# Kernel optimization log

Measured on AMD Instinct MI355X. Metric: run time of the kernel, lower is better.

Reference implementation:

```python
import jax, jax.numpy as jnp
import numpy as np

B, N, K = 4, 1024, 32
C_S, C_Z, C_H, H, PQ, PV = 384, 128, 16, 12, 4, 8
INF, EPS = 1e5, 1e-8
LN_EPS = 1e-5


def _quat_to_rot(q):
    # q: [..., 4] unit quaternions -> [..., 3, 3]
    w, x, y, z = q[..., 0], q[..., 1], q[..., 2], q[..., 3]
    r = jnp.stack([
        1 - 2 * (y * y + z * z), 2 * (x * y - w * z), 2 * (x * z + w * y),
        2 * (x * y + w * z), 1 - 2 * (x * x + z * z), 2 * (y * z - w * x),
        2 * (x * z - w * y), 2 * (y * z + w * x), 1 - 2 * (x * x + y * y),
    ], axis=-1)
    return r.reshape(q.shape[:-1] + (3, 3))


def _layernorm(x, scale, bias):
    m = jnp.mean(x, axis=-1, keepdims=True)
    v = jnp.mean((x - m) ** 2, axis=-1, keepdims=True)
    return (x - m) * jax.lax.rsqrt(v + LN_EPS) * scale + bias


def setup_inputs():
    key = jax.random.key(0)
    ks = jax.random.split(key, 16)
    s = jax.random.normal(ks[0], (B, N, C_S), jnp.float32)
    z = jax.random.normal(ks[1], (B, N, K, C_Z), jnp.float32)
    edge_index = jax.random.randint(ks[2], (B, N, K), 0, N, jnp.int32)
    quat = jax.random.normal(ks[3], (B, N, 4), jnp.float32)
    rot = _quat_to_rot(quat / jnp.linalg.norm(quat, axis=-1, keepdims=True))
    trans = 10.0 * jax.random.normal(ks[4], (B, N, 3), jnp.float32)
    s_mask = jnp.ones((B, N), jnp.float32)
    sc_s, sc_z = C_S ** -0.5, C_Z ** -0.5
    return {
        "s": s, "z": z, "edge_index": edge_index, "rot": rot, "trans": trans,
        "s_mask": s_mask,
        "ln_s_scale": jnp.ones((C_S,), jnp.float32),
        "ln_s_bias": jnp.zeros((C_S,), jnp.float32),
        "ln_z_scale": jnp.ones((C_Z,), jnp.float32),
        "ln_z_bias": jnp.zeros((C_Z,), jnp.float32),
        "w_q": sc_s * jax.random.normal(ks[5], (C_S, H * C_H), jnp.float32),
        "w_k": sc_s * jax.random.normal(ks[6], (C_S, H * C_H), jnp.float32),
        "w_v": sc_s * jax.random.normal(ks[7], (C_S, H * C_H), jnp.float32),
        "w_q_pts": sc_s * jax.random.normal(ks[8], (C_S, H * PQ * 3), jnp.float32),
        "w_kv_pts": sc_s * jax.random.normal(ks[9], (C_S, H * (PQ + PV) * 3), jnp.float32),
        "w_b": sc_z * jax.random.normal(ks[10], (C_Z, H), jnp.float32),
        "w_down_z": sc_z * jax.random.normal(ks[11], (C_Z, C_Z // 4), jnp.float32),
        "head_weights": jnp.full((H,), 0.541324854612918, jnp.float32),  # softplus^-1(1)
        "w_out": (H * 80) ** -0.5 * jax.random.normal(ks[12], (H * (C_Z // 4 + C_H + PV * 4), C_S), jnp.float32),
    }


def reference(s, z, edge_index, rot, trans, s_mask, ln_s_scale, ln_s_bias,
              ln_z_scale, ln_z_bias, w_q, w_k, w_v, w_q_pts, w_kv_pts, w_b,
              w_down_z, head_weights, w_out):
    bidx = jnp.arange(B)[:, None, None]
    s_ln = _layernorm(s, ln_s_scale, ln_s_bias)          # [B,N,C_S]
    z_ln = _layernorm(z, ln_z_scale, ln_z_bias)          # [B,N,K,C_Z]

    q = (s_ln @ w_q).reshape(B, N, H, C_H)
    k = (s_ln @ w_k)[bidx, edge_index].reshape(B, N, K, H, C_H)
    v = (s_ln @ w_v)[bidx, edge_index].reshape(B, N, K, H, C_H)

    # query points in global frame (query residue's rigid)
    q_pts = (s_ln @ w_q_pts).reshape(B, N, H * PQ, 3)
    q_pts = jnp.einsum('bnij,bnpj->bnpi', rot, q_pts) + trans[:, :, None]
    q_pts = q_pts.reshape(B, N, H, PQ, 3)

    # kv points: gather neighbor local points, then (as in source) apply the
    # QUERY residue's rigid r[..., None, None]
    kv = (s_ln @ w_kv_pts)[bidx, edge_index].reshape(B, N, K, H * (PQ + PV), 3)
    kv = jnp.einsum('bnij,bnkpj->bnkpi', rot, kv) + trans[:, :, None, None]
    kv = kv.reshape(B, N, K, H, PQ + PV, 3)
    k_pts, v_pts = kv[..., :PQ, :], kv[..., PQ:, :]

    b_bias = z_ln @ w_b                                   # [B,N,K,H]
    a = jnp.einsum('bnhc,bnkhc->bnkh', q, k) * (1.0 / (3 * C_H)) ** 0.5
    a = a + (1.0 / 3.0) ** 0.5 * b_bias

    disp = q_pts[:, :, None] - k_pts                      # [B,N,K,H,PQ,3]
    sq = jnp.sum(disp * disp, axis=-1)                    # [B,N,K,H,PQ]
    hw = jax.nn.softplus(head_weights) * (1.0 / (3 * (PQ * 9.0 / 2))) ** 0.5
    a = a - 0.5 * jnp.sum(sq * hw[:, None], axis=-1)      # [B,N,K,H]

    m = s_mask[:, :, None] * s_mask[bidx, edge_index]     # [B,N,K]
    a = a + (INF * (m - 1.0))[..., None]

    a = jax.nn.softmax(jnp.swapaxes(a, -1, -2), axis=-1)  # [B,N,H,K]

    o = jnp.einsum('bnhk,bnkhc->bnhc', a, v).reshape(B, N, H * C_H)

    o_pt = jnp.einsum('bnhk,bnkhvc->bnhvc', a, v_pts)     # [B,N,H,PV,3]
    o_pt = jnp.einsum('bnji,bnhvj->bnhvi', rot, o_pt - trans[:, :, None, None])
    dists = jnp.sqrt(jnp.sum(o_pt * o_pt, axis=-1) + EPS).reshape(B, N, H * PV)
    o_pt_flat = o_pt.reshape(B, N, H * PV * 3)

    o_pair = jnp.einsum('bnhk,bnkc->bnhc', a, z_ln @ w_down_z).reshape(B, N, -1)

    out = jnp.concatenate([o, o_pt_flat, dists, o_pair], axis=-1) @ w_out
    return out
```

## Files before the change

### kernel.cpp

```cpp
#include <hip/hip_runtime.h>
#include <hip/hip_bf16.h>

constexpr int Bb = 4, Nn = 1024, Kk = 32;
constexpr int CS = 384, CZ = 128, CH = 16, Hh = 12, PQn = 4, PVn = 8;
constexpr int NCOLS = 1152;
constexpr int FEAT = 960;
constexpr int NNODE = Bb * Nn;
constexpr int NEDGE = NNODE * Kk;
constexpr int ZOC = 44;

constexpr int O_WZP   = 4;
constexpr int O_BVEC  = O_WZP + 6144;
constexpr int O_CSUM  = O_BVEC + 48;
constexpr int O_P     = O_CSUM + 48;
constexpr int O_ZOUT  = O_P + NNODE * NCOLS;
constexpr int O_SLNH  = O_ZOUT + NEDGE * ZOC;
constexpr int O_SLNL  = O_SLNH + NNODE * CS / 2;
constexpr int O_WNTH  = O_SLNL + NNODE * CS / 2;
constexpr int O_WNTL  = O_WNTH + NCOLS * CS / 2;
constexpr int O_WOTH  = O_WNTL + NCOLS * CS / 2;
constexpr int O_WOTL  = O_WOTH + CS * FEAT / 2;
constexpr int O_FEATH = O_SLNH;
constexpr int O_FEATL = O_WOTL + CS * FEAT / 2;
constexpr int TOTAL_F = O_FEATL + NNODE * FEAT / 2;

typedef __attribute__((ext_vector_type(8)))  short short8x;
typedef __attribute__((ext_vector_type(16))) float f32x16;

__device__ __forceinline__ float ldf(const float* p, int i) { return p[i]; }
__device__ __forceinline__ float ldf(const __hip_bfloat16* p, int i) { return __bfloat162float(p[i]); }
__device__ __forceinline__ void stf(float* p, size_t i, float v) { p[i] = v; }
__device__ __forceinline__ void stf(__hip_bfloat16* p, size_t i, float v) { p[i] = __float2bfloat16(v); }
__device__ __forceinline__ float4 ld4(const float* p, int i) { return *(const float4*)(p + i); }
__device__ __forceinline__ float4 ld4(const __hip_bfloat16* p, int i) {
    ushort4 u = *(const ushort4*)(p + i);
    return make_float4(__uint_as_float((unsigned)u.x << 16),
                       __uint_as_float((unsigned)u.y << 16),
                       __uint_as_float((unsigned)u.z << 16),
                       __uint_as_float((unsigned)u.w << 16));
}
__device__ __forceinline__ void split_bf(float v, unsigned short& h, unsigned short& l) {
    h = (unsigned short)(__float_as_uint(v) >> 16);
    float r = v - __uint_as_float((unsigned)h << 16);
    l = (unsigned short)(__float_as_uint(r) >> 16);
}

__global__ void k_detect(const unsigned* smask_raw, int* flag) {
    if (threadIdx.x == 0) *flag = (smask_raw[0] == 0x3F803F80u) ? 1 : 0;
}

template <typename T>
__global__ __launch_bounds__(384) void k_prep(const T* s, const T* lns_sc, const T* lns_bi,
                                              const T* wq, const T* wk, const T* wv,
                                              const T* wqp, const T* wkvp, const T* wout,
                                              const T* wb, const T* wdz, const T* zsc, const T* zbi,
                                              float* wsf, const int* flag, int want) {
    if (flag && *flag != want) return;
    int blk = blockIdx.x, t = threadIdx.x;
    unsigned short* wntH = (unsigned short*)(wsf + O_WNTH);
    unsigned short* wntL = (unsigned short*)(wsf + O_WNTL);
    unsigned short* wotH = (unsigned short*)(wsf + O_WOTH);
    unsigned short* wotL = (unsigned short*)(wsf + O_WOTL);
    unsigned short* slnH = (unsigned short*)(wsf + O_SLNH);
    unsigned short* slnL = (unsigned short*)(wsf + O_SLNL);
    __shared__ float ssum[6], ssq[6];
    if (blk < 1152) {
        int n = blk, k = t;
        float v;
        if      (n < 192) v = ldf(wq,  k * 192 + n);
        else if (n < 384) v = ldf(wk,  k * 192 + n - 192);
        else if (n < 576) v = ldf(wv,  k * 192 + n - 384);
        else if (n < 720) v = ldf(wqp, k * 144 + n - 576);
        else              v = ldf(wkvp, k * 432 + n - 720);
        unsigned short h, l; split_bf(v, h, l);
        wntH[n * 384 + k] = h; wntL[n * 384 + k] = l;
    } else if (blk < 1536) {
        int n = blk - 1152;
        for (int k = t; k < 960; k += 384) {
            float v = ldf(wout, k * 384 + n);
            unsigned short h, l; split_bf(v, h, l);
            wotH[n * 960 + k] = h; wotL[n * 960 + k] = l;
        }
    } else if (blk < 1536 + 4096) {
        int row = blk - 1536;
        float x = ldf(s, row * CS + t);
        float sum = x, sq = x * x;
        #pragma unroll
        for (int m = 32; m; m >>= 1) { sum += __shfl_xor(sum, m, 64); sq += __shfl_xor(sq, m, 64); }
        int w = t >> 6;
        if ((t & 63) == 0) { ssum[w] = sum; ssq[w] = sq; }
        __syncthreads();
        if (t == 0) {
            float S = 0, Q = 0;
            for (int i = 0; i < 6; i++) { S += ssum[i]; Q += ssq[i]; }
            ssum[0] = S; ssq[0] = Q;
        }
        __syncthreads();
        float mean = ssum[0] * (1.f / CS);
        float var  = ssq[0] * (1.f / CS) - mean * mean;
        float r = rsqrtf(var + 1e-5f);
        float y = (x - mean) * r * ldf(lns_sc, t) + ldf(lns_bi, t);
        unsigned short h, l; split_bf(y, h, l);
        slnH[row * CS + t] = h; slnL[row * CS + t] = l;
    } else {
        if (t < 128) {
            float sc = ldf(zsc, t);
            for (int o = 0; o < 48; o++) {
                float w = 0.f;
                if (o < 12)      w = ldf(wb, t * 12 + o);
                else if (o < 44) w = ldf(wdz, t * 32 + o - 12);
                wsf[O_WZP + t * 48 + o] = sc * w;
            }
        } else if (t < 176) {
            int o = t - 128;
            float acc = 0.f;
            if (o < 44)
                for (int c = 0; c < 128; c++)
                    acc += ldf(zbi, c) * (o < 12 ? ldf(wb, c * 12 + o) : ldf(wdz, c * 32 + o - 12));
            wsf[O_BVEC + o] = acc;
        } else if (t < 224) {
            int o = t - 176;
            float acc = 0.f;
            if (o < 44)
                for (int c = 0; c < 128; c++)
                    acc += ldf(zsc, c) * (o < 12 ? ldf(wb, c * 12 + o) : ldf(wdz, c * 32 + o - 12));
            wsf[O_CSUM + o] = acc;
        }
    }
}

template <typename T>
__global__ __launch_bounds__(256) void k_zg(const T* z, const float* wzp, const float* bvec,
                                            const float* csum, float* zout,
                                            const int* flag, int want) {
    if (flag && *flag != want) return;
    __shared__ float Ws[128 * 48];
    __shared__ float As[16][260];
    __shared__ float mus[256], rss[256];
    int t = threadIdx.x;
    int edge0 = blockIdx.x * 256;
    for (int i = t; i < 128 * 48; i += 256) Ws[i] = wzp[i];
    int tm = t >> 2, tn = t & 3, col = tn * 12;
    int sr = t >> 2, q = t & 3;
    float psum[4] = {}, psq[4] = {};
    float acc[4][12] = {};
    for (int kt = 0; kt < CZ; kt += 16) {
        float4 zv[4];
        #pragma unroll
        for (int u = 0; u < 4; u++) {
            zv[u] = ld4(z, (edge0 + sr + 64 * u) * CZ + kt + q * 4);
            psum[u] += zv[u].x + zv[u].y + zv[u].z + zv[u].w;
            psq[u]  += zv[u].x * zv[u].x + zv[u].y * zv[u].y
                     + zv[u].z * zv[u].z + zv[u].w * zv[u].w;
        }
        __syncthreads();
        #pragma unroll
        for (int u = 0; u < 4; u++) {
            int rr = sr + 64 * u;
            As[q * 4 + 0][rr] = zv[u].x;
            As[q * 4 + 1][rr] = zv[u].y;
            As[q * 4 + 2][rr] = zv[u].z;
            As[q * 4 + 3][rr] = zv[u].w;
        }
        __syncthreads();
        #pragma unroll
        for (int kk = 0; kk < 16; kk++) {
            float4 a = *(const float4*)&As[kk][tm * 4];
            const float* wr = &Ws[(kt + kk) * 48 + col];
            float4 b0 = *(const float4*)(wr);
            float4 b1 = *(const float4*)(wr + 4);
            float4 b2 = *(const float4*)(wr + 8);
            float av[4]  = {a.x, a.y, a.z, a.w};
            float bv[12] = {b0.x, b0.y, b0.z, b0.w, b1.x, b1.y, b1.z, b1.w, b2.x, b2.y, b2.z, b2.w};
            #pragma unroll
            for (int i = 0; i < 4; i++)
                #pragma unroll
                for (int j = 0; j < 12; j++) acc[i][j] += av[i] * bv[j];
        }
        __syncthreads();
    }
    #pragma unroll
    for (int u = 0; u < 4; u++) {
        float s = psum[u], qq = psq[u];
        s += __shfl_xor(s, 1, 64); s += __shfl_xor(s, 2, 64);
        qq += __shfl_xor(qq, 1, 64); qq += __shfl_xor(qq, 2, 64);
        if (q == 0) {
            float mu = s * (1.f / CZ);
            mus[sr + 64 * u] = mu;
            rss[sr + 64 * u] = rsqrtf(qq * (1.f / CZ) - mu * mu + 1e-5f);
        }
    }
    __syncthreads();
    #pragma unroll
    for (int i = 0; i < 4; i++) {
        int r = tm * 4 + i;
        float mu = mus[r], rs = rss[r];
        int e = edge0 + r;
        #pragma unroll
        for (int j = 0; j < 12; j++) {
            int c = col + j;
            if (c < ZOC) zout[(size_t)e * ZOC + c] = rs * acc[i][j] - rs * mu * csum[c] + bvec[c];
        }
    }
}

#define MFMA3(C, AH, AL, BH, BL)                                              \
    C = __builtin_amdgcn_mfma_f32_32x32x16_bf16(AH, BH, C, 0, 0, 0);          \
    C = __builtin_amdgcn_mfma_f32_32x32x16_bf16(AH, BL, C, 0, 0, 0);          \
    C = __builtin_amdgcn_mfma_f32_32x32x16_bf16(AL, BH, C, 0, 0, 0);

template <typename TO>
__global__ __launch_bounds__(64) void k_mgemm(const unsigned short* AH, const unsigned short* AL,
                                              int lda, const unsigned short* BH,
                                              const unsigned short* BL, int ldb,
                                              TO* C, int ldc, int Kdim,
                                              const int* flag, int want) {
    if (flag && *flag != want) return;
    int l = threadIdx.x, r = l & 31, g = l >> 5;
    size_t a0 = (size_t)(blockIdx.x * 64 + r) * lda + 8 * g;
    size_t a1 = a0 + (size_t)32 * lda;
    size_t b0 = (size_t)(blockIdx.y * 64 + r) * ldb + 8 * g;
    size_t b1 = b0 + (size_t)32 * ldb;
    f32x16 c00 = {}, c01 = {}, c10 = {}, c11 = {};
    short8x aH0 = *(const short8x*)(AH + a0), aH1 = *(const short8x*)(AH + a1);
    short8x aL0 = *(const short8x*)(AL + a0), aL1 = *(const short8x*)(AL + a1);
    short8x bH0 = *(const short8x*)(BH + b0), bH1 = *(const short8x*)(BH + b1);
    short8x bL0 = *(const short8x*)(BL + b0), bL1 = *(const short8x*)(BL + b1);
    for (int kt = 0; kt < Kdim; kt += 16) {
        int kn = (kt + 16 < Kdim) ? kt + 16 : 0;
        short8x nAH0 = *(const short8x*)(AH + a0 + kn), nAH1 = *(const short8x*)(AH + a1 + kn);
        short8x nAL0 = *(const short8x*)(AL + a0 + kn), nAL1 = *(const short8x*)(AL + a1 + kn);
        short8x nBH0 = *(const short8x*)(BH + b0 + kn), nBH1 = *(const short8x*)(BH + b1 + kn);
        short8x nBL0 = *(const short8x*)(BL + b0 + kn), nBL1 = *(const short8x*)(BL + b1 + kn);
        MFMA3(c00, aH0, aL0, bH0, bL0)
        MFMA3(c01, aH0, aL0, bH1, bL1)
        MFMA3(c10, aH1, aL1, bH0, bL0)
        MFMA3(c11, aH1, aL1, bH1, bL1)
        aH0 = nAH0; aH1 = nAH1; aL0 = nAL0; aL1 = nAL1;
        bH0 = nBH0; bH1 = nBH1; bL0 = nBL0; bL1 = nBL1;
    }
    #pragma unroll
    for (int reg = 0; reg < 16; reg++) {
        int row = (reg & 3) + 8 * (reg >> 2) + 4 * g;
        size_t rm = (size_t)(blockIdx.x * 64 + row);
        int cn = blockIdx.y * 64 + r;
        stf(C, rm * ldc + cn,               c00[reg]);
        stf(C, rm * ldc + cn + 32,          c01[reg]);
        stf(C, (rm + 32) * ldc + cn,        c10[reg]);
        stf(C, (rm + 32) * ldc + cn + 32,   c11[reg]);
    }
}

template <typename T>
__global__ __launch_bounds__(256) void k_attn(const float* P, const float* zout,
                                              const int* eidx, const T* smask, const T* rot,
                                              const T* hwq, unsigned short* featH,
                                              unsigned short* featL, const int* flag, int want) {
    if (flag && *flag != want) return;
    __shared__ float nds[4][1760];
    __shared__ int js[4][32];
    int bid = blockIdx.x;
    int nb = ((bid & 7) << 7) + (bid >> 3);
    int w = threadIdx.x >> 6, lane = threadIdx.x & 63;
    int node = nb * 4 + w;
    int b = node >> 10;
    float* S = nds[w];
    int* J = js[w];
    const float* Pn = P + (size_t)node * NCOLS;
    for (int u = lane; u < 336; u += 64)
        S[u] = (u < 192) ? Pn[u] : Pn[384 + u];
    if (lane < 32) {
        int j = eidx[node * Kk + lane];
        J[lane] = b * Nn + j;
        S[360 + lane] = ldf(smask, node) * ldf(smask, b * Nn + j);
    } else if (lane < 44) {
        int h = lane - 32;
        float x = ldf(hwq, h);
        S[336 + h] = logf(1.f + expf(x)) * 0.13608276348795434f;
    } else if (lane < 53) {
        int u = lane - 44;
        int i = u / 3, jj = u - i * 3;
        float m = 0;
        #pragma unroll
        for (int l = 0; l < 3; l++)
            m += ldf(rot, node * 9 + l * 3 + i) * ldf(rot, node * 9 + l * 3 + jj);
        S[348 + u] = m;
    }
    __builtin_amdgcn_wave_barrier();
    #pragma unroll
    for (int it = 0; it < 6; it++) {
        int u = lane + 64 * it;
        int h = u >> 5, k = u & 31;
        const float* Pj = P + (size_t)J[k] * NCOLS;
        float qk = 0;
        const float4* pk4 = (const float4*)(Pj + 192 + h * 16);
        const float4* qs4 = (const float4*)(S + h * 16);
        #pragma unroll
        for (int c4 = 0; c4 < 4; c4++) {
            float4 pv = pk4[c4], qv = qs4[c4];
            qk += qv.x * pv.x + qv.y * pv.y + qv.z * pv.z + qv.w * pv.w;
        }
        float M00 = S[348], M01 = S[349], M02 = S[350],
              M11 = S[352], M12 = S[353], M22 = S[356];
        const float4* pp4 = (const float4*)(Pj + 720 + h * 36);
        const float4* qp4 = (const float4*)(S + 192 + h * 12);
        float4 A0 = pp4[0], A1 = pp4[1], A2 = pp4[2];
        float4 B0 = qp4[0], B1 = qp4[1], B2 = qp4[2];
        float d[12] = {B0.x - A0.x, B0.y - A0.y, B0.z - A0.z, B0.w - A0.w,
                       B1.x - A1.x, B1.y - A1.y, B1.z - A1.z, B1.w - A1.w,
                       B2.x - A2.x, B2.y - A2.y, B2.z - A2.z, B2.w - A2.w};
        float sq = 0;
        #pragma unroll
        for (int p = 0; p < 4; p++) {
            float d0 = d[p * 3], d1 = d[p * 3 + 1], d2 = d[p * 3 + 2];
            sq += M00 * d0 * d0 + M11 * d1 * d1 + M22 * d2 * d2
                + 2.f * (M01 * d0 * d1 + M02 * d0 * d2 + M12 * d1 * d2);
        }
        float logit = qk * 0.14433756729740643f
                    + 0.5773502691896258f * zout[((size_t)node * Kk + k) * ZOC + h]
                    - 0.5f * S[336 + h] * sq
                    + 1e5f * (S[360 + k] - 1.f);
        float mx = logit;
        #pragma unroll
        for (int m = 16; m; m >>= 1) mx = fmaxf(mx, __shfl_xor(mx, m, 64));
        float e = expf(logit - mx);
        float ssum = e;
        #pragma unroll
        for (int m = 16; m; m >>= 1) ssum += __shfl_xor(ssum, m, 64);
        S[392 + h * 33 + k] = e / ssum;
    }
    __builtin_amdgcn_wave_barrier();
    for (int u = lane; u < 216; u += 64) {
        int h, off, fbase, pair = 0;
        if (u < 48)       { h = u >> 2; off = 384 + h * 16 + (u & 3) * 4; fbase = h * 16 + (u & 3) * 4; }
        else if (u < 120) { int v = u - 48;  h = v / 6; int q = v - h * 6;
                            off = 732 + h * 36 + q * 4; fbase = 192 + h * 24 + q * 4; }
        else              { int v = u - 120; h = v >> 3;
                            off = 12 + (v & 7) * 4; fbase = 576 + h * 32 + (v & 7) * 4; pair = 1; }
        float4 acc = {0.f, 0.f, 0.f, 0.f};
        const float* lrow = S + 392 + h * 33;
        if (!pair) {
            #pragma unroll 8
            for (int k = 0; k < 32; k++) {
                float lw = lrow[k];
                float4 pv = *(const float4*)(P + (size_t)J[k] * NCOLS + off);
                acc.x += lw * pv.x; acc.y += lw * pv.y; acc.z += lw * pv.z; acc.w += lw * pv.w;
            }
        } else {
            const float* zr = zout + (size_t)node * Kk * ZOC + off;
            #pragma unroll 8
            for (int k = 0; k < 32; k++) {
                float lw = lrow[k];
                float4 pv = *(const float4*)(zr + k * ZOC);
                acc.x += lw * pv.x; acc.y += lw * pv.y; acc.z += lw * pv.z; acc.w += lw * pv.w;
            }
        }
        *(float4*)&S[788 + fbase] = acc;
    }
    __builtin_amdgcn_wave_barrier();
    for (int u = lane; u < 96; u += 64) {
        float r0 = S[788 + 192 + u * 3 + 0];
        float r1 = S[788 + 192 + u * 3 + 1];
        float r2 = S[788 + 192 + u * 3 + 2];
        float o0 = S[348] * r0 + S[349] * r1 + S[350] * r2;
        float o1 = S[351] * r0 + S[352] * r1 + S[353] * r2;
        float o2 = S[354] * r0 + S[355] * r1 + S[356] * r2;
        S[788 + 192 + u * 3 + 0] = o0;
        S[788 + 192 + u * 3 + 1] = o1;
        S[788 + 192 + u * 3 + 2] = o2;
        S[788 + 480 + u] = sqrtf(o0 * o0 + o1 * o1 + o2 * o2 + 1e-8f);
    }
    __builtin_amdgcn_wave_barrier();
    for (int u = lane; u < FEAT; u += 64) {
        unsigned short h, l; split_bf(S[788 + u], h, l);
        featH[(size_t)node * FEAT + u] = h;
        featL[(size_t)node * FEAT + u] = l;
    }
}

extern "C" void kernel_launch(void* const* d_in, const int* in_sizes, int n_in,
                              void* d_out, int out_size, void* d_ws, size_t ws_size,
                              hipStream_t stream) {
    float* wsf = (float*)d_ws;
    int* flag = (int*)d_ws;
    const void* s = d_in[0];   const void* z = d_in[1];
    const int* eidx = (const int*)d_in[2];
    const void* rot = d_in[3];
    const void* smask = d_in[5];
    const void* lns_sc = d_in[6]; const void* lns_bi = d_in[7];
    const void* lnz_sc = d_in[8]; const void* lnz_bi = d_in[9];
    const void* wq = d_in[10]; const void* wk = d_in[11]; const void* wv = d_in[12];
    const void* wqp = d_in[13]; const void* wkvp = d_in[14];
    const void* wb = d_in[15]; const void* wdz = d_in[16];
    const void* hwq = d_in[17]; const void* wout = d_in[18];

    unsigned short* slnH = (unsigned short*)(wsf + O_SLNH);
    unsigned short* slnL = (unsigned short*)(wsf + O_SLNL);
    unsigned short* wntH = (unsigned short*)(wsf + O_WNTH);
    unsigned short* wntL = (unsigned short*)(wsf + O_WNTL);
    unsigned short* wotH = (unsigned short*)(wsf + O_WOTH);
    unsigned short* wotL = (unsigned short*)(wsf + O_WOTL);
    unsigned short* featH = (unsigned short*)(wsf + O_FEATH);
    unsigned short* featL = (unsigned short*)(wsf + O_FEATL);

    int mode = -1;
    if (in_sizes) {
        if (in_sizes[0] == NNODE * CS * 4) mode = 0;
        else if (in_sizes[0] == NNODE * CS * 2) mode = 1;
    }
    const int* fg = (mode < 0) ? flag : nullptr;
    if (mode < 0) k_detect<<<1, 64, 0, stream>>>((const unsigned*)smask, flag);

    #define LAUNCH_FRONT(T, WANT)                                                                 \
        do {                                                                                      \
            k_prep<T><<<5633, 384, 0, stream>>>((const T*)s, (const T*)lns_sc, (const T*)lns_bi,  \
                (const T*)wq, (const T*)wk, (const T*)wv, (const T*)wqp, (const T*)wkvp,          \
                (const T*)wout, (const T*)wb, (const T*)wdz, (const T*)lnz_sc, (const T*)lnz_bi,  \
                wsf, fg, WANT);                                                                   \
            k_zg<T><<<NEDGE / 256, 256, 0, stream>>>((const T*)z, wsf + O_WZP, wsf + O_BVEC,      \
                wsf + O_CSUM, wsf + O_ZOUT, fg, WANT);                                            \
        } while (0)

    #define LAUNCH_ATTN(T, WANT)                                                                  \
        k_attn<T><<<NNODE / 4, 256, 0, stream>>>(wsf + O_P, wsf + O_ZOUT, eidx,                   \
            (const T*)smask, (const T*)rot, (const T*)hwq, featH, featL, fg, WANT)

    if (mode == 0)      LAUNCH_FRONT(float, 0);
    else if (mode == 1) LAUNCH_FRONT(__hip_bfloat16, 1);
    else { LAUNCH_FRONT(float, 0); LAUNCH_FRONT(__hip_bfloat16, 1); }

    k_mgemm<float><<<dim3(NNODE / 64, NCOLS / 64), 64, 0, stream>>>(
        slnH, slnL, CS, wntH, wntL, CS, wsf + O_P, NCOLS, CS, nullptr, 0);

    if (mode == 0) {
        LAUNCH_ATTN(float, 0);
        k_mgemm<float><<<dim3(NNODE / 64, CS / 64), 64, 0, stream>>>(
            featH, featL, FEAT, wotH, wotL, FEAT, (float*)d_out, CS, FEAT, nullptr, 0);
    } else if (mode == 1) {
        LAUNCH_ATTN(__hip_bfloat16, 1);
        k_mgemm<__hip_bfloat16><<<dim3(NNODE / 64, CS / 64), 64, 0, stream>>>(
            featH, featL, FEAT, wotH, wotL, FEAT, (__hip_bfloat16*)d_out, CS, FEAT, nullptr, 0);
    } else {
        LAUNCH_ATTN(float, 0);
        LAUNCH_ATTN(__hip_bfloat16, 1);
        k_mgemm<float><<<dim3(NNODE / 64, CS / 64), 64, 0, stream>>>(
            featH, featL, FEAT, wotH, wotL, FEAT, (float*)d_out, CS, FEAT, fg, 0);
        k_mgemm<__hip_bfloat16><<<dim3(NNODE / 64, CS / 64), 64, 0, stream>>>(
            featH, featL, FEAT, wotH, wotL, FEAT, (__hip_bfloat16*)d_out, CS, FEAT, fg, 1);
    }
    #undef LAUNCH_FRONT
    #undef LAUNCH_ATTN
}
```

Baseline: 345.9 us.

## Fuse pipeline stages into one cooperative persistent kernel with grid syncs

Replaces the five separate launches (prep, z layernorm-GEMM, input GEMM, attention, output GEMM) with a single cooperative kernel of 1024 blocks that runs each stage and separates them with grid-wide syncs. Work is redistributed so that each stage fits 1024 blocks of 256 threads: the z GEMM processes 128 edges per block, the prep stage is remapped to 256-thread virtual blocks, and each wave computes one GEMM tile. The GEMM also drops its register double-buffer prefetch. The intent is to remove launch gaps and tail effects. The costs are fewer waves in flight for the small GEMMs and grid-sync stalls, with a fallback to separate launches if the cooperative launch fails.

```diff
diff --git a/kernel.cpp b/kernel.cpp
--- a/kernel.cpp
+++ b/kernel.cpp
@@ -1,5 +1,8 @@
 #include <hip/hip_runtime.h>
 #include <hip/hip_bf16.h>
+#include <hip/hip_cooperative_groups.h>
+
+namespace cg = cooperative_groups;
 
 constexpr int Bb = 4, Nn = 1024, Kk = 32;
 constexpr int CS = 384, CZ = 128, CH = 16, Hh = 12, PQn = 4, PVn = 8;
@@ -8,6 +11,7 @@
 constexpr int NNODE = Bb * Nn;
 constexpr int NEDGE = NNODE * Kk;
 constexpr int ZOC = 44;
+constexpr int NPREP = 1728 + 1440 + 1024 + 1;
 
 constexpr int O_WZP   = 4;
 constexpr int O_BVEC  = O_WZP + 6144;
@@ -31,8 +35,8 @@
 __device__ __forceinline__ float ldf(const __hip_bfloat16* p, int i) { return __bfloat162float(p[i]); }
 __device__ __forceinline__ void stf(float* p, size_t i, float v) { p[i] = v; }
 __device__ __forceinline__ void stf(__hip_bfloat16* p, size_t i, float v) { p[i] = __float2bfloat16(v); }
-__device__ __forceinline__ float4 ld4(const float* p, int i) { return *(const float4*)(p + i); }
-__device__ __forceinline__ float4 ld4(const __hip_bfloat16* p, int i) {
+__device__ __forceinline__ float4 ld4(const float* p, size_t i) { return *(const float4*)(p + i); }
+__device__ __forceinline__ float4 ld4(const __hip_bfloat16* p, size_t i) {
     ushort4 u = *(const ushort4*)(p + i);
     return make_float4(__uint_as_float((unsigned)u.x << 16),
                        __uint_as_float((unsigned)u.y << 16),
@@ -50,22 +54,20 @@
 }
 
 template <typename T>
-__global__ __launch_bounds__(384) void k_prep(const T* s, const T* lns_sc, const T* lns_bi,
-                                              const T* wq, const T* wk, const T* wv,
-                                              const T* wqp, const T* wkvp, const T* wout,
-                                              const T* wb, const T* wdz, const T* zsc, const T* zbi,
-                                              float* wsf, const int* flag, int want) {
-    if (flag && *flag != want) return;
-    int blk = blockIdx.x, t = threadIdx.x;
+__device__ __forceinline__ void dev_prep(int vb, int t,
+    const T* s, const T* lns_sc, const T* lns_bi,
+    const T* wq, const T* wk, const T* wv, const T* wqp, const T* wkvp, const T* wout,
+    const T* wb, const T* wdz, const T* zsc, const T* zbi, float* wsf)
+{
     unsigned short* wntH = (unsigned short*)(wsf + O_WNTH);
     unsigned short* wntL = (unsigned short*)(wsf + O_WNTL);
     unsigned short* wotH = (unsigned short*)(wsf + O_WOTH);
     unsigned short* wotL = (unsigned short*)(wsf + O_WOTL);
     unsigned short* slnH = (unsigned short*)(wsf + O_SLNH);
     unsigned short* slnL = (unsigned short*)(wsf + O_SLNL);
-    __shared__ float ssum[6], ssq[6];
-    if (blk < 1152) {
-        int n = blk, k = t;
+    if (vb < 1728) {
+        int idx = vb * 256 + t;
+        int n = idx / 384, k = idx - n * 384;
         float v;
         if      (n < 192) v = ldf(wq,  k * 192 + n);
         else if (n < 384) v = ldf(wk,  k * 192 + n - 192);
@@ -74,34 +76,32 @@
         else              v = ldf(wkvp, k * 432 + n - 720);
         unsigned short h, l; split_bf(v, h, l);
         wntH[n * 384 + k] = h; wntL[n * 384 + k] = l;
-    } else if (blk < 1536) {
-        int n = blk - 1152;
-        for (int k = t; k < 960; k += 384) {
-            float v = ldf(wout, k * 384 + n);
-            unsigned short h, l; split_bf(v, h, l);
-            wotH[n * 960 + k] = h; wotL[n * 960 + k] = l;
-        }
-    } else if (blk < 1536 + 4096) {
-        int row = blk - 1536;
-        float x = ldf(s, row * CS + t);
-        float sum = x, sq = x * x;
+    } else if (vb < 3168) {
+        int idx = (vb - 1728) * 256 + t;
+        int n = idx / 960, k = idx - n * 960;
+        float v = ldf(wout, k * 384 + n);
+        unsigned short h, l; split_bf(v, h, l);
+        wotH[n * 960 + k] = h; wotL[n * 960 + k] = l;
+    } else if (vb < 4192) {
+        int row = (vb - 3168) * 4 + (t >> 6), lane = t & 63;
+        float x[6]; float sum = 0, sq = 0;
+        #pragma unroll
+        for (int j = 0; j < 6; j++) {
+            float v = ldf(s, row * CS + lane + 64 * j);
+            x[j] = v; sum += v; sq += v * v;
+        }
         #pragma unroll
         for (int m = 32; m; m >>= 1) { sum += __shfl_xor(sum, m, 64); sq += __shfl_xor(sq, m, 64); }
-        int w = t >> 6;
-        if ((t & 63) == 0) { ssum[w] = sum; ssq[w] = sq; }
-        __syncthreads();
-        if (t == 0) {
-            float S = 0, Q = 0;
-            for (int i = 0; i < 6; i++) { S += ssum[i]; Q += ssq[i]; }
-            ssum[0] = S; ssq[0] = Q;
-        }
-        __syncthreads();
-        float mean = ssum[0] * (1.f / CS);
-        float var  = ssq[0] * (1.f / CS) - mean * mean;
+        float mean = sum * (1.f / CS);
+        float var  = sq * (1.f / CS) - mean * mean;
         float r = rsqrtf(var + 1e-5f);
-        float y = (x - mean) * r * ldf(lns_sc, t) + ldf(lns_bi, t);
-        unsigned short h, l; split_bf(y, h, l);
-        slnH[row * CS + t] = h; slnL[row * CS + t] = l;
+        #pragma unroll
+        for (int j = 0; j < 6; j++) {
+            int c = lane + 64 * j;
+            float y = (x[j] - mean) * r * ldf(lns_sc, c) + ldf(lns_bi, c);
+            unsigned short h, l; split_bf(y, h, l);
+            slnH[(size_t)row * CS + c] = h; slnL[(size_t)row * CS + c] = l;
+        }
     } else {
         if (t < 128) {
             float sc = ldf(zsc, t);
@@ -130,78 +130,67 @@
 }
 
 template <typename T>
-__global__ __launch_bounds__(256) void k_zg(const T* z, const float* wzp, const float* bvec,
-                                            const float* csum, float* zout,
-                                            const int* flag, int want) {
-    if (flag && *flag != want) return;
-    __shared__ float Ws[128 * 48];
-    __shared__ float As[16][260];
-    __shared__ float mus[256], rss[256];
-    int t = threadIdx.x;
-    int edge0 = blockIdx.x * 256;
-    for (int i = t; i < 128 * 48; i += 256) Ws[i] = wzp[i];
-    int tm = t >> 2, tn = t & 3, col = tn * 12;
-    int sr = t >> 2, q = t & 3;
-    float psum[4] = {}, psq[4] = {};
-    float acc[4][12] = {};
+__device__ void dev_zg(int vb, int t, const T* z, const float* wzp, const float* bvec,
+                       const float* csum, float* zout, float* sm)
+{
+    float* Ws  = sm;
+    float* Asf = sm + 6144;
+    float* mus = sm + 6144 + 2112;
+    float* rss = mus + 128;
+    int edge0 = vb * 128;
+    for (int i = t; i < 6144; i += 256) Ws[i] = wzp[i];
+    int sr = t >> 1, q = t & 1;
+    int r0 = (t >> 2) * 2, col = (t & 3) * 12;
+    float psum = 0, psq = 0;
+    float acc[2][12] = {};
     for (int kt = 0; kt < CZ; kt += 16) {
-        float4 zv[4];
-        #pragma unroll
-        for (int u = 0; u < 4; u++) {
-            zv[u] = ld4(z, (edge0 + sr + 64 * u) * CZ + kt + q * 4);
-            psum[u] += zv[u].x + zv[u].y + zv[u].z + zv[u].w;
-            psq[u]  += zv[u].x * zv[u].x + zv[u].y * zv[u].y
-                     + zv[u].z * zv[u].z + zv[u].w * zv[u].w;
-        }
+        float4 z0 = ld4(z, (size_t)(edge0 + sr) * CZ + kt + q * 8);
+        float4 z1 = ld4(z, (size_t)(edge0 + sr) * CZ + kt + q * 8 + 4);
+        psum += z0.x + z0.y + z0.z + z0.w + z1.x + z1.y + z1.z + z1.w;
+        psq  += z0.x*z0.x + z0.y*z0.y + z0.z*z0.z + z0.w*z0.w
+              + z1.x*z1.x + z1.y*z1.y + z1.z*z1.z + z1.w*z1.w;
         __syncthreads();
-        #pragma unroll
-        for (int u = 0; u < 4; u++) {
-            int rr = sr + 64 * u;
-            As[q * 4 + 0][rr] = zv[u].x;
-            As[q * 4 + 1][rr] = zv[u].y;
-            As[q * 4 + 2][rr] = zv[u].z;
-            As[q * 4 + 3][rr] = zv[u].w;
-        }
+        Asf[(q * 8 + 0) * 132 + sr] = z0.x;
+        Asf[(q * 8 + 1) * 132 + sr] = z0.y;
+        Asf[(q * 8 + 2) * 132 + sr] = z0.z;
+        Asf[(q * 8 + 3) * 132 + sr] = z0.w;
+        Asf[(q * 8 + 4) * 132 + sr] = z1.x;
+        Asf[(q * 8 + 5) * 132 + sr] = z1.y;
+        Asf[(q * 8 + 6) * 132 + sr] = z1.z;
+        Asf[(q * 8 + 7) * 132 + sr] = z1.w;
         __syncthreads();
         #pragma unroll
         for (int kk = 0; kk < 16; kk++) {
-            float4 a = *(const float4*)&As[kk][tm * 4];
+            float a0 = Asf[kk * 132 + r0], a1 = Asf[kk * 132 + r0 + 1];
             const float* wr = &Ws[(kt + kk) * 48 + col];
             float4 b0 = *(const float4*)(wr);
             float4 b1 = *(const float4*)(wr + 4);
             float4 b2 = *(const float4*)(wr + 8);
-            float av[4]  = {a.x, a.y, a.z, a.w};
-            float bv[12] = {b0.x, b0.y, b0.z, b0.w, b1.x, b1.y, b1.z, b1.w, b2.x, b2.y, b2.z, b2.w};
+            float bv[12] = {b0.x,b0.y,b0.z,b0.w,b1.x,b1.y,b1.z,b1.w,b2.x,b2.y,b2.z,b2.w};
             #pragma unroll
-            for (int i = 0; i < 4; i++)
-                #pragma unroll
-                for (int j = 0; j < 12; j++) acc[i][j] += av[i] * bv[j];
-        }
-        __syncthreads();
-    }
-    #pragma unroll
-    for (int u = 0; u < 4; u++) {
-        float s = psum[u], qq = psq[u];
-        s += __shfl_xor(s, 1, 64); s += __shfl_xor(s, 2, 64);
-        qq += __shfl_xor(qq, 1, 64); qq += __shfl_xor(qq, 2, 64);
-        if (q == 0) {
-            float mu = s * (1.f / CZ);
-            mus[sr + 64 * u] = mu;
-            rss[sr + 64 * u] = rsqrtf(qq * (1.f / CZ) - mu * mu + 1e-5f);
-        }
+            for (int j = 0; j < 12; j++) { acc[0][j] += a0 * bv[j]; acc[1][j] += a1 * bv[j]; }
+        }
+    }
+    psum += __shfl_xor(psum, 1, 64);
+    psq  += __shfl_xor(psq, 1, 64);
+    if (q == 0) {
+        float mu = psum * (1.f / CZ);
+        mus[sr] = mu;
+        rss[sr] = rsqrtf(psq * (1.f / CZ) - mu * mu + 1e-5f);
     }
     __syncthreads();
     #pragma unroll
-    for (int i = 0; i < 4; i++) {
-        int r = tm * 4 + i;
+    for (int i = 0; i < 2; i++) {
+        int r = r0 + i;
         float mu = mus[r], rs = rss[r];
-        int e = edge0 + r;
+        size_t e = edge0 + r;
         #pragma unroll
         for (int j = 0; j < 12; j++) {
             int c = col + j;
-            if (c < ZOC) zout[(size_t)e * ZOC + c] = rs * acc[i][j] - rs * mu * csum[c] + bvec[c];
-        }
-    }
+            if (c < ZOC) zout[e * ZOC + c] = rs * acc[i][j] - rs * mu * csum[c] + bvec[c];
+        }
+    }
+    __syncthreads();
 }
 
 #define MFMA3(C, AH, AL, BH, BL)                                              \
@@ -210,62 +199,51 @@
     C = __builtin_amdgcn_mfma_f32_32x32x16_bf16(AL, BH, C, 0, 0, 0);
 
 template <typename TO>
-__global__ __launch_bounds__(64) void k_mgemm(const unsigned short* AH, const unsigned short* AL,
-                                              int lda, const unsigned short* BH,
-                                              const unsigned short* BL, int ldb,
-                                              TO* C, int ldc, int Kdim,
-                                              const int* flag, int want) {
-    if (flag && *flag != want) return;
-    int l = threadIdx.x, r = l & 31, g = l >> 5;
-    size_t a0 = (size_t)(blockIdx.x * 64 + r) * lda + 8 * g;
+__device__ void dev_mgemm_tile(int bx, int by, int l,
+                               const unsigned short* AH, const unsigned short* AL, int lda,
+                               const unsigned short* BH, const unsigned short* BL, int ldb,
+                               TO* C, int ldc, int Kdim)
+{
+    int r = l & 31, g = l >> 5;
+    size_t a0 = (size_t)(bx * 64 + r) * lda + 8 * g;
     size_t a1 = a0 + (size_t)32 * lda;
-    size_t b0 = (size_t)(blockIdx.y * 64 + r) * ldb + 8 * g;
+    size_t b0 = (size_t)(by * 64 + r) * ldb + 8 * g;
     size_t b1 = b0 + (size_t)32 * ldb;
     f32x16 c00 = {}, c01 = {}, c10 = {}, c11 = {};
-    short8x aH0 = *(const short8x*)(AH + a0), aH1 = *(const short8x*)(AH + a1);
-    short8x aL0 = *(const short8x*)(AL + a0), aL1 = *(const short8x*)(AL + a1);
-    short8x bH0 = *(const short8x*)(BH + b0), bH1 = *(const short8x*)(BH + b1);
-    short8x bL0 = *(const short8x*)(BL + b0), bL1 = *(const short8x*)(BL + b1);
     for (int kt = 0; kt < Kdim; kt += 16) {
-        int kn = (kt + 16 < Kdim) ? kt + 16 : 0;
-        short8x nAH0 = *(const short8x*)(AH + a0 + kn), nAH1 = *(const short8x*)(AH + a1 + kn);
-        short8x nAL0 = *(const short8x*)(AL + a0 + kn), nAL1 = *(const short8x*)(AL + a1 + kn);
-        short8x nBH0 = *(const short8x*)(BH + b0 + kn), nBH1 = *(const short8x*)(BH + b1 + kn);
-        short8x nBL0 = *(const short8x*)(BL + b0 + kn), nBL1 = *(const short8x*)(BL + b1 + kn);
+        short8x aH0 = *(const short8x*)(AH + a0 + kt), aH1 = *(const short8x*)(AH + a1 + kt);
+        short8x aL0 = *(const short8x*)(AL + a0 + kt), aL1 = *(const short8x*)(AL + a1 + kt);
+        short8x bH0 = *(const short8x*)(BH + b0 + kt), bH1 = *(const short8x*)(BH + b1 + kt);
+        short8x bL0 = *(const short8x*)(BL + b0 + kt), bL1 = *(const short8x*)(BL + b1 + kt);
         MFMA3(c00, aH0, aL0, bH0, bL0)
         MFMA3(c01, aH0, aL0, bH1, bL1)
         MFMA3(c10, aH1, aL1, bH0, bL0)
         MFMA3(c11, aH1, aL1, bH1, bL1)
-        aH0 = nAH0; aH1 = nAH1; aL0 = nAL0; aL1 = nAL1;
-        bH0 = nBH0; bH1 = nBH1; bL0 = nBL0; bL1 = nBL1;
     }
     #pragma unroll
     for (int reg = 0; reg < 16; reg++) {
         int row = (reg & 3) + 8 * (reg >> 2) + 4 * g;
-        size_t rm = (size_t)(blockIdx.x * 64 + row);
-        int cn = blockIdx.y * 64 + r;
-        stf(C, rm * ldc + cn,               c00[reg]);
-        stf(C, rm * ldc + cn + 32,          c01[reg]);
-        stf(C, (rm + 32) * ldc + cn,        c10[reg]);
-        stf(C, (rm + 32) * ldc + cn + 32,   c11[reg]);
+        size_t rm = (size_t)(bx * 64 + row);
+        int cn = by * 64 + r;
+        stf(C, rm * ldc + cn,             c00[reg]);
+        stf(C, rm * ldc + cn + 32,        c01[reg]);
+        stf(C, (rm + 32) * ldc + cn,      c10[reg]);
+        stf(C, (rm + 32) * ldc + cn + 32, c11[reg]);
     }
 }
 
 template <typename T>
-__global__ __launch_bounds__(256) void k_attn(const float* P, const float* zout,
-                                              const int* eidx, const T* smask, const T* rot,
-                                              const T* hwq, unsigned short* featH,
-                                              unsigned short* featL, const int* flag, int want) {
-    if (flag && *flag != want) return;
-    __shared__ float nds[4][1760];
-    __shared__ int js[4][32];
-    int bid = blockIdx.x;
+__device__ void dev_attn(int bid, int t, float* smAll, int* jsAll,
+                         const float* P, const float* zout, const int* eidx,
+                         const T* smask, const T* rot, const T* hwq,
+                         unsigned short* featH, unsigned short* featL)
+{
     int nb = ((bid & 7) << 7) + (bid >> 3);
-    int w = threadIdx.x >> 6, lane = threadIdx.x & 63;
+    int w = t >> 6, lane = t & 63;
     int node = nb * 4 + w;
     int b = node >> 10;
-    float* S = nds[w];
-    int* J = js[w];
+    float* S = smAll + w * 1760;
+    int* J = jsAll + w * 32;
     const float* Pn = P + (size_t)node * NCOLS;
     for (int u = lane; u < 336; u += 64)
         S[u] = (u < 192) ? Pn[u] : Pn[384 + u];
@@ -282,8 +260,8 @@
         int i = u / 3, jj = u - i * 3;
         float m = 0;
         #pragma unroll
-        for (int l = 0; l < 3; l++)
-            m += ldf(rot, node * 9 + l * 3 + i) * ldf(rot, node * 9 + l * 3 + jj);
+        for (int l2 = 0; l2 < 3; l2++)
+            m += ldf(rot, node * 9 + l2 * 3 + i) * ldf(rot, node * 9 + l2 * 3 + jj);
         S[348 + u] = m;
     }
     __builtin_amdgcn_wave_barrier();
@@ -378,6 +356,139 @@
     }
 }
 
+template <typename T, typename TO>
+__global__ __launch_bounds__(256, 4) void k_fused(const T* s, const T* z, const int* eidx,
+    const T* rot, const T* smask, const T* lns_sc, const T* lns_bi,
+    const T* wq, const T* wk, const T* wv, const T* wqp, const T* wkvp,
+    const T* wb, const T* wdz, const T* zsc, const T* zbi, const T* hwq, const T* wout,
+    float* wsf, TO* out)
+{
+    __shared__ float sm[8512];
+    __shared__ int js[4][32];
+    cg::grid_group gg = cg::this_grid();
+    int bid = blockIdx.x, t = threadIdx.x;
+
+    for (int vb = bid; vb < NPREP; vb += 1024)
+        dev_prep<T>(vb, t, s, lns_sc, lns_bi, wq, wk, wv, wqp, wkvp, wout, wb, wdz, zsc, zbi, wsf);
+    gg.sync();
+
+    dev_zg<T>(bid, t, z, wsf + O_WZP, wsf + O_BVEC, wsf + O_CSUM, wsf + O_ZOUT, sm);
+    gg.sync();
+
+    const unsigned short* slnH = (const unsigned short*)(wsf + O_SLNH);
+    const unsigned short* slnL = (const unsigned short*)(wsf + O_SLNL);
+    const unsigned short* wntH = (const unsigned short*)(wsf + O_WNTH);
+    const unsigned short* wntL = (const unsigned short*)(wsf + O_WNTL);
+    const unsigned short* wotH = (const unsigned short*)(wsf + O_WOTH);
+    const unsigned short* wotL = (const unsigned short*)(wsf + O_WOTL);
+    unsigned short* featH = (unsigned short*)(wsf + O_FEATH);
+    unsigned short* featL = (unsigned short*)(wsf + O_FEATL);
+
+    {
+        int w = t >> 6, lane = t & 63;
+        int wid = bid * 4 + w;
+        for (int tile = wid; tile < 64 * 18; tile += 4096)
+            dev_mgemm_tile<float>(tile & 63, tile >> 6, lane, slnH, slnL, CS, wntH, wntL, CS,
+                                  wsf + O_P, NCOLS, CS);
+    }
+    gg.sync();
+
+    dev_attn<T>(bid, t, sm, &js[0][0], wsf + O_P, wsf + O_ZOUT, eidx, smask, rot, hwq, featH, featL);
+    gg.sync();
+
+    {
+        int w = t >> 6, lane = t & 63;
+        int wid = bid * 4 + w;
+        for (int tile = wid; tile < 64 * 6; tile += 4096)
+            dev_mgemm_tile<TO>(tile & 63, tile >> 6, lane, featH, featL, FEAT, wotH, wotL, FEAT,
+                               out, CS, FEAT);
+    }
+}
+
+template <typename T>
+__global__ __launch_bounds__(256) void k_prep_s(const T* s, const T* lns_sc, const T* lns_bi,
+    const T* wq, const T* wk, const T* wv, const T* wqp, const T* wkvp, const T* wout,
+    const T* wb, const T* wdz, const T* zsc, const T* zbi, float* wsf, const int* flag, int want) {
+    if (flag && *flag != want) return;
+    dev_prep<T>(blockIdx.x, threadIdx.x, s, lns_sc, lns_bi, wq, wk, wv, wqp, wkvp, wout,
+                wb, wdz, zsc, zbi, wsf);
+}
+
+template <typename T>
+__global__ __launch_bounds__(256) void k_zg_s(const T* z, const float* wzp, const float* bvec,
+    const float* csum, float* zout, const int* flag, int want) {
+    if (flag && *flag != want) return;
+    __shared__ float sm[8512];
+    dev_zg<T>(blockIdx.x, threadIdx.x, z, wzp, bvec, csum, zout, sm);
+}
+
+template <typename TO>
+__global__ __launch_bounds__(64) void k_mgemm_s(const unsigned short* AH, const unsigned short* AL,
+    int lda, const unsigned short* BH, const unsigned short* BL, int ldb,
+    TO* C, int ldc, int Kdim, const int* flag, int want) {
+    if (flag && *flag != want) return;
+    dev_mgemm_tile<TO>(blockIdx.x, blockIdx.y, threadIdx.x, AH, AL, lda, BH, BL, ldb, C, ldc, Kdim);
+}
+
+template <typename T>
+__global__ __launch_bounds__(256) void k_attn_s(const float* P, const float* zout, const int* eidx,
+    const T* smask, const T* rot, const T* hwq, unsigned short* featH, unsigned short* featL,
+    const int* flag, int want) {
+    if (flag && *flag != want) return;
+    __shared__ float sm[7040];
+    __shared__ int js[4][32];
+    dev_attn<T>(blockIdx.x, threadIdx.x, sm, &js[0][0], P, zout, eidx, smask, rot, hwq, featH, featL);
+}
+
+template <typename T, typename TO>
+static void run_path(const void* s, const void* z, const int* eidx, const void* rot,
+                     const void* smask, const void* lns_sc, const void* lns_bi,
+                     const void* wq, const void* wk, const void* wv, const void* wqp,
+                     const void* wkvp, const void* wb, const void* wdz, const void* zsc,
+                     const void* zbi, const void* hwq, const void* wout,
+                     float* wsf, void* dout, const int* fg, int want, bool try_coop,
+                     hipStream_t stream)
+{
+    unsigned short* slnH = (unsigned short*)(wsf + O_SLNH);
+    unsigned short* slnL = (unsigned short*)(wsf + O_SLNL);
+    unsigned short* wntH = (unsigned short*)(wsf + O_WNTH);
+    unsigned short* wntL = (unsigned short*)(wsf + O_WNTL);
+    unsigned short* wotH = (unsigned short*)(wsf + O_WOTH);
+    unsigned short* wotL = (unsigned short*)(wsf + O_WOTL);
+    unsigned short* featH = (unsigned short*)(wsf + O_FEATH);
+    unsigned short* featL = (unsigned short*)(wsf + O_FEATL);
+
+    if (try_coop) {
+        const T *sP = (const T*)s, *zP = (const T*)z, *rotP = (const T*)rot,
+                *smP = (const T*)smask, *lsP = (const T*)lns_sc, *lbP = (const T*)lns_bi,
+                *wqP = (const T*)wq, *wkP = (const T*)wk, *wvP = (const T*)wv,
+                *wqpP = (const T*)wqp, *wkvpP = (const T*)wkvp, *wbP = (const T*)wb,
+                *wdzP = (const T*)wdz, *zscP = (const T*)zsc, *zbiP = (const T*)zbi,
+                *hwqP = (const T*)hwq, *woP = (const T*)wout;
+        const int* eP = eidx;
+        float* wsP = wsf;
+        TO* oP = (TO*)dout;
+        void* prm[20] = {&sP, &zP, &eP, &rotP, &smP, &lsP, &lbP, &wqP, &wkP, &wvP,
+                         &wqpP, &wkvpP, &wbP, &wdzP, &zscP, &zbiP, &hwqP, &woP, &wsP, &oP};
+        hipError_t err = hipLaunchCooperativeKernel(
+            reinterpret_cast<void*>(&k_fused<T, TO>), dim3(1024), dim3(256), prm, 0, stream);
+        if (err == hipSuccess) return;
+        (void)hipGetLastError();
+    }
+
+    k_prep_s<T><<<NPREP, 256, 0, stream>>>((const T*)s, (const T*)lns_sc, (const T*)lns_bi,
+        (const T*)wq, (const T*)wk, (const T*)wv, (const T*)wqp, (const T*)wkvp,
+        (const T*)wout, (const T*)wb, (const T*)wdz, (const T*)zsc, (const T*)zbi, wsf, fg, want);
+    k_zg_s<T><<<1024, 256, 0, stream>>>((const T*)z, wsf + O_WZP, wsf + O_BVEC, wsf + O_CSUM,
+        wsf + O_ZOUT, fg, want);
+    k_mgemm_s<float><<<dim3(64, 18), 64, 0, stream>>>(slnH, slnL, CS, wntH, wntL, CS,
+        wsf + O_P, NCOLS, CS, (const int*)nullptr, 0);
+    k_attn_s<T><<<1024, 256, 0, stream>>>(wsf + O_P, wsf + O_ZOUT, eidx, (const T*)smask,
+        (const T*)rot, (const T*)hwq, featH, featL, fg, want);
+    k_mgemm_s<TO><<<dim3(64, 6), 64, 0, stream>>>(featH, featL, FEAT, wotH, wotL, FEAT,
+        (TO*)dout, CS, FEAT, fg, want);
+}
+
 extern "C" void kernel_launch(void* const* d_in, const int* in_sizes, int n_in,
                               void* d_out, int out_size, void* d_ws, size_t ws_size,
                               hipStream_t stream) {
@@ -394,60 +505,27 @@
     const void* wb = d_in[15]; const void* wdz = d_in[16];
     const void* hwq = d_in[17]; const void* wout = d_in[18];
 
-    unsigned short* slnH = (unsigned short*)(wsf + O_SLNH);
-    unsigned short* slnL = (unsigned short*)(wsf + O_SLNL);
-    unsigned short* wntH = (unsigned short*)(wsf + O_WNTH);
-    unsigned short* wntL = (unsigned short*)(wsf + O_WNTL);
-    unsigned short* wotH = (unsigned short*)(wsf + O_WOTH);
-    unsigned short* wotL = (unsigned short*)(wsf + O_WOTL);
-    unsigned short* featH = (unsigned short*)(wsf + O_FEATH);
-    unsigned short* featL = (unsigned short*)(wsf + O_FEATL);
-
     int mode = -1;
     if (in_sizes) {
         if (in_sizes[0] == NNODE * CS * 4) mode = 0;
         else if (in_sizes[0] == NNODE * CS * 2) mode = 1;
     }
-    const int* fg = (mode < 0) ? flag : nullptr;
-    if (mode < 0) k_detect<<<1, 64, 0, stream>>>((const unsigned*)smask, flag);
-
-    #define LAUNCH_FRONT(T, WANT)                                                                 \
-        do {                                                                                      \
-            k_prep<T><<<5633, 384, 0, stream>>>((const T*)s, (const T*)lns_sc, (const T*)lns_bi,  \
-                (const T*)wq, (const T*)wk, (const T*)wv, (const T*)wqp, (const T*)wkvp,          \
-                (const T*)wout, (const T*)wb, (const T*)wdz, (const T*)lnz_sc, (const T*)lnz_bi,  \
-                wsf, fg, WANT);                                                                   \
-            k_zg<T><<<NEDGE / 256, 256, 0, stream>>>((const T*)z, wsf + O_WZP, wsf + O_BVEC,      \
-                wsf + O_CSUM, wsf + O_ZOUT, fg, WANT);                                            \
-        } while (0)
-
-    #define LAUNCH_ATTN(T, WANT)                                                                  \
-        k_attn<T><<<NNODE / 4, 256, 0, stream>>>(wsf + O_P, wsf + O_ZOUT, eidx,                   \
-            (const T*)smask, (const T*)rot, (const T*)hwq, featH, featL, fg, WANT)
-
-    if (mode == 0)      LAUNCH_FRONT(float, 0);
-    else if (mode == 1) LAUNCH_FRONT(__hip_bfloat16, 1);
-    else { LAUNCH_FRONT(float, 0); LAUNCH_FRONT(__hip_bfloat16, 1); }
-
-    k_mgemm<float><<<dim3(NNODE / 64, NCOLS / 64), 64, 0, stream>>>(
-        slnH, slnL, CS, wntH, wntL, CS, wsf + O_P, NCOLS, CS, nullptr, 0);
 
     if (mode == 0) {
-        LAUNCH_ATTN(float, 0);
-        k_mgemm<float><<<dim3(NNODE / 64, CS / 64), 64, 0, stream>>>(
-            featH, featL, FEAT, wotH, wotL, FEAT, (float*)d_out, CS, FEAT, nullptr, 0);
+        run_path<float, float>(s, z, eidx, rot, smask, lns_sc, lns_bi, wq, wk, wv, wqp, wkvp,
+                               wb, wdz, lnz_sc, lnz_bi, hwq, wout, wsf, d_out,
+                               nullptr, 0, true, stream);
     } else if (mode == 1) {
-        LAUNCH_ATTN(__hip_bfloat16, 1);
-        k_mgemm<__hip_bfloat16><<<dim3(NNODE / 64, CS / 64), 64, 0, stream>>>(
-            featH, featL, FEAT, wotH, wotL, FEAT, (__hip_bfloat16*)d_out, CS, FEAT, nullptr, 0);
+        run_path<__hip_bfloat16, __hip_bfloat16>(s, z, eidx, rot, smask, lns_sc, lns_bi,
+                               wq, wk, wv, wqp, wkvp, wb, wdz, lnz_sc, lnz_bi, hwq, wout,
+                               wsf, d_out, nullptr, 0, true, stream);
     } else {
-        LAUNCH_ATTN(float, 0);
-        LAUNCH_ATTN(__hip_bfloat16, 1);
-        k_mgemm<float><<<dim3(NNODE / 64, CS / 64), 64, 0, stream>>>(
-            featH, featL, FEAT, wotH, wotL, FEAT, (float*)d_out, CS, FEAT, fg, 0);
-        k_mgemm<__hip_bfloat16><<<dim3(NNODE / 64, CS / 64), 64, 0, stream>>>(
-            featH, featL, FEAT, wotH, wotL, FEAT, (__hip_bfloat16*)d_out, CS, FEAT, fg, 1);
-    }
-    #undef LAUNCH_FRONT
-    #undef LAUNCH_ATTN
-}
+        k_detect<<<1, 64, 0, stream>>>((const unsigned*)smask, flag);
+        run_path<float, float>(s, z, eidx, rot, smask, lns_sc, lns_bi, wq, wk, wv, wqp, wkvp,
+                               wb, wdz, lnz_sc, lnz_bi, hwq, wout, wsf, d_out,
+                               flag, 0, false, stream);
+        run_path<__hip_bfloat16, __hip_bfloat16>(s, z, eidx, rot, smask, lns_sc, lns_bi,
+                               wq, wk, wv, wqp, wkvp, wb, wdz, lnz_sc, lnz_bi, hwq, wout,
+                               wsf, d_out, flag, 1, false, stream);
+    }
+}
```

Result: slower. 405.2 us (+17.1%).
